# Performance work log

Measured on AMD Instinct MI355X. Metric: run time of the kernel, lower is better.

## Reference

```python
import jax, jax.numpy as jnp
import numpy as np

B, T, I, H, O, L = 128, 1024, 256, 512, 256, 2


def setup_inputs() -> dict:
    key = jax.random.key(0)
    ks = jax.random.split(key, 12)
    s_in = 1.0 / np.sqrt(I)
    s_h = 1.0 / np.sqrt(H)
    return {
        "x": jax.random.normal(ks[0], (B, T, I), dtype=jnp.float32),
        "h0": jax.random.normal(ks[1], (B, H), dtype=jnp.float32),
        # layer 0: input_size -> hidden
        "W_ih0": jax.random.uniform(ks[2], (H, I), jnp.float32, -s_in, s_in),
        "b_ih0": jax.random.uniform(ks[3], (H,), jnp.float32, -s_in, s_in),
        "W_hh0": jax.random.uniform(ks[4], (H, H), jnp.float32, -s_h, s_h),
        "b_hh0": jax.random.uniform(ks[5], (H,), jnp.float32, -s_h, s_h),
        # layer 1: hidden -> hidden
        "W_ih1": jax.random.uniform(ks[6], (H, H), jnp.float32, -s_h, s_h),
        "b_ih1": jax.random.uniform(ks[7], (H,), jnp.float32, -s_h, s_h),
        "W_hh1": jax.random.uniform(ks[8], (H, H), jnp.float32, -s_h, s_h),
        "b_hh1": jax.random.uniform(ks[9], (H,), jnp.float32, -s_h, s_h),
        # output head
        "W_out": jax.random.uniform(ks[10], (O, H), jnp.float32, -s_h, s_h),
        "b_out": jax.random.uniform(ks[11], (O,), jnp.float32, -s_h, s_h),
    }


def reference(x, h0, W_ih0, b_ih0, W_hh0, b_hh0, W_ih1, b_ih1, W_hh1, b_hh1, W_out, b_out):
    """Returns Y: (B, T, O). Single hidden state h threaded through all layers,
    matching the original module's loop structure."""
    layers = ((W_ih0, b_ih0, W_hh0, b_hh0), (W_ih1, b_ih1, W_hh1, b_hh1))

    def step(h, x_t):  # h: (B,H), x_t: (B,I)
        inp = x_t
        for (Wih, bih, Whh, bhh) in layers:
            h = jnp.tanh(inp @ Wih.T + bih + h @ Whh.T + bhh)
            inp = h
        y = inp @ W_out.T + b_out  # (B, O)
        return h, y

    xs = jnp.swapaxes(x, 0, 1)  # (T, B, I)
    _, ys = jax.lax.scan(step, h0, xs)
    return jnp.swapaxes(ys, 0, 1)  # (B, T, O)
```

## Files before the change

kernel.cpp:

```cpp
#include <hip/hip_runtime.h>
#include <cstdint>
#include <cstddef>


typedef _Float16 f16;
typedef _Float16 f16x8 __attribute__((ext_vector_type(8)));
typedef float    f32x4 __attribute__((ext_vector_type(4)));

#define NB 128
#define NT 1024
#define NI 256
#define NH 512
#define NO 256
#define RD 4

#define WS_WHH0 (size_t)(0)
#define WS_W1C  (size_t)(524288)
#define WS_WOUT (size_t)(1048576)
#define WS_WIH0 (size_t)(1310720)
#define WS_BC0  (size_t)(1572864)
#define WS_B1C  (size_t)(1574912)
#define WS_BOUT (size_t)(1576960)
#define WS_H1R  (size_t)(2097152)
#define WS_H2R  (size_t)(2621440)
#define WS_FLG  (size_t)(3145728)

#define AGENT __HIP_MEMORY_SCOPE_AGENT

__device__ __forceinline__ f32x4 mfma16(f16x8 a, f16x8 b, f32x4 c) {
  return __builtin_amdgcn_mfma_f32_16x16x32_f16(a, b, c, 0, 0, 0);
}

__device__ __forceinline__ float fast_tanh(float v) {
  float a = __builtin_fabsf(v);
  float e = __expf(-2.0f * a);
  float r = (1.0f - e) * __builtin_amdgcn_rcpf(1.0f + e);
  return v < 0.0f ? -r : r;
}

__device__ __forceinline__ void poll4(int* base, int target) {
  for (;;) {
    int a = __hip_atomic_load(base,      __ATOMIC_RELAXED, AGENT);
    int b = __hip_atomic_load(base + 16, __ATOMIC_RELAXED, AGENT);
    int c = __hip_atomic_load(base + 32, __ATOMIC_RELAXED, AGENT);
    int d = __hip_atomic_load(base + 48, __ATOMIC_RELAXED, AGENT);
    if (a >= target && b >= target && c >= target && d >= target) return;
    __builtin_amdgcn_s_sleep(2);
  }
}

__global__ __launch_bounds__(256) void rnn9277_prep(
    const float* __restrict__ h0,
    const float* __restrict__ Wih0, const float* __restrict__ bih0,
    const float* __restrict__ Whh0, const float* __restrict__ bhh0,
    const float* __restrict__ Wih1, const float* __restrict__ bih1,
    const float* __restrict__ Whh1, const float* __restrict__ bhh1,
    const float* __restrict__ Woutp, const float* __restrict__ boutp,
    char* __restrict__ ws)
{
  const int tid = blockIdx.x * 256 + threadIdx.x;
  const int stride = gridDim.x * 256;
  f16* whh0 = (f16*)(ws + WS_WHH0);
  f16* w1c  = (f16*)(ws + WS_W1C);
  f16* wout = (f16*)(ws + WS_WOUT);
  f16* wih0 = (f16*)(ws + WS_WIH0);
  float* bc0 = (float*)(ws + WS_BC0);
  float* b1c = (float*)(ws + WS_B1C);
  float* bo  = (float*)(ws + WS_BOUT);
  uint64_t* h2r64 = (uint64_t*)(ws + WS_H2R);
  int* h1f = (int*)(ws + WS_FLG);
  int* h2f = (int*)(ws + WS_FLG + 2048);

  for (int i = tid; i < NH * NH; i += stride) whh0[i] = (f16)Whh0[i];
  for (int i = tid; i < NH * NH; i += stride) w1c[i]  = (f16)(Wih1[i] + Whh1[i]);
  for (int i = tid; i < NO * NH; i += stride) wout[i] = (f16)Woutp[i];
  for (int i = tid; i < NH * NI; i += stride) wih0[i] = (f16)Wih0[i];
  for (int i = tid; i < NH; i += stride) { bc0[i] = bih0[i] + bhh0[i]; b1c[i] = bih1[i] + bhh1[i]; }
  for (int i = tid; i < NO; i += stride) bo[i] = boutp[i];
  for (int c = tid; c < NB * NH / 4; c += stride) {
    int b = c >> 7, c4 = c & 127;
    int g = b >> 4, bl = b & 15;
    const float* hp = h0 + (size_t)b * NH + c4 * 4;
    union { uint64_t u; f16 h[4]; } uv;
    uv.h[0] = (f16)hp[0]; uv.h[1] = (f16)hp[1]; uv.h[2] = (f16)hp[2]; uv.h[3] = (f16)hp[3];
    __hip_atomic_store(h2r64 + (size_t)(g * RD + 3) * 2048 + bl * 128 + c4, uv.u,
                       __ATOMIC_RELAXED, AGENT);
  }
  if (tid < 32) {
    __hip_atomic_store(h1f + tid * 16, 0, __ATOMIC_RELAXED, AGENT);
    __hip_atomic_store(h2f + tid * 16, 0, __ATOMIC_RELAXED, AGENT);
  }
}

__global__ __launch_bounds__(512) void rnn9277_chain(
    const float* __restrict__ x, float* __restrict__ out, char* __restrict__ ws)
{
  const int wg = blockIdx.x;
  const bool isL0 = wg < 32;
  const int g = (wg & 31) >> 2, j = wg & 3;
  const int tid = threadIdx.x;
  const int wave = tid >> 6, lane = tid & 63;
  const int row16 = lane & 15, kq = lane >> 4;

  const f16* whh0 = (const f16*)(ws + WS_WHH0);
  const f16* w1c  = (const f16*)(ws + WS_W1C);
  const f16* wout = (const f16*)(ws + WS_WOUT);
  const f16* wih0 = (const f16*)(ws + WS_WIH0);
  const float* bc0 = (const float*)(ws + WS_BC0);
  const float* b1c = (const float*)(ws + WS_B1C);
  const float* bo  = (const float*)(ws + WS_BOUT);
  uint64_t* h1r64 = (uint64_t*)(ws + WS_H1R);
  uint64_t* h2r64 = (uint64_t*)(ws + WS_H2R);
  int* h1fb = (int*)(ws + WS_FLG) + g * 64;
  int* h2fb = (int*)(ws + WS_FLG + 2048) + g * 64;

  __shared__ __align__(16) f16 stage[2][16 * 520];
  __shared__ __align__(16) f16 xpose[16 * 136];

  f16x8 Bh[16];
  f16x8 Bx[8];
  f16x8 By[16];
  float bias = 0.f, ybias = 0.f;
  {
    const int col = j * 128 + wave * 16 + row16;
    const f16* wp = (isL0 ? whh0 : w1c) + (size_t)col * NH + kq * 8;
    #pragma unroll
    for (int kk = 0; kk < 16; kk++) Bh[kk] = *(const f16x8*)(wp + kk * 32);
    bias = (isL0 ? bc0 : b1c)[col];
    if (isL0) {
      const f16* qp = wih0 + (size_t)col * NI + kq * 8;
      #pragma unroll
      for (int kk = 0; kk < 8; kk++) Bx[kk] = *(const f16x8*)(qp + kk * 32);
      if (wave < 4) {
        const int oc = j * 64 + wave * 16 + row16;
        const f16* rp = wout + (size_t)oc * NH + kq * 8;
        #pragma unroll
        for (int kk = 0; kk < 16; kk++) By[kk] = *(const f16x8*)(rp + kk * 32);
        ybias = bo[oc];
      }
    }
  }

  if (isL0) {
    for (int t = 0; t <= NT; ++t) {
      f32x4 acc = {0.f, 0.f, 0.f, 0.f};
      if (t < NT) {
        const float* xp = x + ((size_t)(g * 16 + row16) * NT + t) * NI + kq * 8;
        #pragma unroll
        for (int kk = 0; kk < 8; kk++) {
          f32x4 lo = *(const f32x4*)(xp + kk * 32);
          f32x4 hi = *(const f32x4*)(xp + kk * 32 + 4);
          f16x8 a;
          a[0] = (f16)lo[0]; a[1] = (f16)lo[1]; a[2] = (f16)lo[2]; a[3] = (f16)lo[3];
          a[4] = (f16)hi[0]; a[5] = (f16)hi[1]; a[6] = (f16)hi[2]; a[7] = (f16)hi[3];
          acc = mfma16(a, Bx[kk], acc);
        }
      }
      if (tid < 64) poll4(h2fb, t);
      __syncthreads();
      const uint64_t* rs = h2r64 + (size_t)(g * RD + ((t + 3) & 3)) * 2048;
      f16* st = &stage[t & 1][0];
      #pragma unroll
      for (int i = 0; i < 4; ++i) {
        int c = tid + i * 512;
        int r = c >> 7, c4 = c & 127;
        uint64_t v = __hip_atomic_load(rs + c, __ATOMIC_RELAXED, AGENT);
        *(uint64_t*)(st + r * 520 + c4 * 4) = v;
      }
      __syncthreads();

      const f16* ap = st + row16 * 520 + kq * 8;
      if (t < NT) {
        #pragma unroll
        for (int kk = 0; kk < 16; kk++)
          acc = mfma16(*(const f16x8*)(ap + kk * 32), Bh[kk], acc);
        const int cl = wave * 16 + row16;
        #pragma unroll
        for (int rr = 0; rr < 4; rr++)
          xpose[(kq * 4 + rr) * 136 + cl] = (f16)fast_tanh(acc[rr] + bias);
        __syncthreads();
        {
          int r = tid >> 5, c4 = tid & 31;
          uint64_t v = *(const uint64_t*)(xpose + r * 136 + c4 * 4);
          __hip_atomic_store(h1r64 + (size_t)(g * RD + (t & 3)) * 2048 + r * 128 + j * 32 + c4,
                             v, __ATOMIC_RELAXED, AGENT);
        }
        __syncthreads();
        if (tid == 0)
          __hip_atomic_store(h1fb + j * 16, t + 1, __ATOMIC_RELAXED, AGENT);
      }
      if (t > 0 && wave < 4) {
        f32x4 ya = {0.f, 0.f, 0.f, 0.f};
        #pragma unroll
        for (int kk = 0; kk < 16; kk++)
          ya = mfma16(*(const f16x8*)(ap + kk * 32), By[kk], ya);
        const int oc = j * 64 + wave * 16 + row16;
        #pragma unroll
        for (int rr = 0; rr < 4; rr++)
          out[((size_t)(g * 16 + kq * 4 + rr) * NT + (t - 1)) * NO + oc] = ya[rr] + ybias;
      }
    }
  } else {
    for (int t = 0; t < NT; ++t) {
      if (tid < 64) poll4(h1fb, t + 1);
      __syncthreads();
      const uint64_t* rs = h1r64 + (size_t)(g * RD + (t & 3)) * 2048;
      f16* st = &stage[t & 1][0];
      #pragma unroll
      for (int i = 0; i < 4; ++i) {
        int c = tid + i * 512;
        int r = c >> 7, c4 = c & 127;
        uint64_t v = __hip_atomic_load(rs + c, __ATOMIC_RELAXED, AGENT);
        *(uint64_t*)(st + r * 520 + c4 * 4) = v;
      }
      __syncthreads();

      const f16* ap = st + row16 * 520 + kq * 8;
      f32x4 acc = {0.f, 0.f, 0.f, 0.f};
      #pragma unroll
      for (int kk = 0; kk < 16; kk++)
        acc = mfma16(*(const f16x8*)(ap + kk * 32), Bh[kk], acc);
      const int cl = wave * 16 + row16;
      #pragma unroll
      for (int rr = 0; rr < 4; rr++)
        xpose[(kq * 4 + rr) * 136 + cl] = (f16)fast_tanh(acc[rr] + bias);
      __syncthreads();
      {
        int r = tid >> 5, c4 = tid & 31;
        uint64_t v = *(const uint64_t*)(xpose + r * 136 + c4 * 4);
        __hip_atomic_store(h2r64 + (size_t)(g * RD + (t & 3)) * 2048 + r * 128 + j * 32 + c4,
                           v, __ATOMIC_RELAXED, AGENT);
      }
      __syncthreads();
      if (tid == 0)
        __hip_atomic_store(h2fb + j * 16, t + 1, __ATOMIC_RELAXED, AGENT);
    }
  }
}

extern "C" void kernel_launch(void* const* d_in, const int* in_sizes, int n_in,
                              void* d_out, int out_size, void* d_ws, size_t ws_size,
                              hipStream_t stream) {
  const float* x    = (const float*)d_in[0];
  const float* h0   = (const float*)d_in[1];
  const float* Wih0 = (const float*)d_in[2];
  const float* bih0 = (const float*)d_in[3];
  const float* Whh0 = (const float*)d_in[4];
  const float* bhh0 = (const float*)d_in[5];
  const float* Wih1 = (const float*)d_in[6];
  const float* bih1 = (const float*)d_in[7];
  const float* Whh1 = (const float*)d_in[8];
  const float* bhh1 = (const float*)d_in[9];
  const float* Wout = (const float*)d_in[10];
  const float* bout = (const float*)d_in[11];
  char* ws = (char*)d_ws;
  float* out = (float*)d_out;

  rnn9277_prep<<<dim3(128), dim3(256), 0, stream>>>(
      h0, Wih0, bih0, Whh0, bhh0, Wih1, bih1, Whh1, bhh1, Wout, bout, ws);
  rnn9277_chain<<<dim3(64), dim3(512), 0, stream>>>(x, out, ws);
}
```

Measured before the change: 6.251 ms.

## Replace flag-based handoff with tag-embedded hidden-state panels and per-thread polling

```diff
diff --git a/kernel.cpp b/kernel.cpp
--- a/kernel.cpp
+++ b/kernel.cpp
@@ -12,7 +12,6 @@
 #define NI 256
 #define NH 512
 #define NO 256
-#define RD 4
 
 #define WS_WHH0 (size_t)(0)
 #define WS_W1C  (size_t)(524288)
@@ -21,11 +20,11 @@
 #define WS_BC0  (size_t)(1572864)
 #define WS_B1C  (size_t)(1574912)
 #define WS_BOUT (size_t)(1576960)
-#define WS_H1R  (size_t)(2097152)
-#define WS_H2R  (size_t)(2621440)
-#define WS_FLG  (size_t)(3145728)
+#define WS_H1P  (size_t)(2097152)
+#define WS_H2P  (size_t)(2621440)
 
 #define AGENT __HIP_MEMORY_SCOPE_AGENT
+#define SPIN_BUDGET (1 << 24)
 
 __device__ __forceinline__ f32x4 mfma16(f16x8 a, f16x8 b, f32x4 c) {
   return __builtin_amdgcn_mfma_f32_16x16x32_f16(a, b, c, 0, 0, 0);
@@ -38,14 +37,25 @@
   return v < 0.0f ? -r : r;
 }
 
-__device__ __forceinline__ void poll4(int* base, int target) {
+__device__ __forceinline__ uint32_t pack_h(float v, uint32_t tag) {
+  union { f16 h; uint16_t u; } cv;
+  cv.h = (f16)v;
+  return ((uint32_t)cv.u << 16) | tag;
+}
+
+__device__ __forceinline__ void poll16(uint32_t* __restrict__ panel, int tid,
+                                       uint32_t expect, uint32_t w[16],
+                                       int* budget) {
   for (;;) {
-    int a = __hip_atomic_load(base,      __ATOMIC_RELAXED, AGENT);
-    int b = __hip_atomic_load(base + 16, __ATOMIC_RELAXED, AGENT);
-    int c = __hip_atomic_load(base + 32, __ATOMIC_RELAXED, AGENT);
-    int d = __hip_atomic_load(base + 48, __ATOMIC_RELAXED, AGENT);
-    if (a >= target && b >= target && c >= target && d >= target) return;
-    __builtin_amdgcn_s_sleep(2);
+    bool ok = true;
+    #pragma unroll
+    for (int i = 0; i < 16; i++) ok &= ((w[i] & 0xFFFFu) == expect);
+    if (ok) return;
+    if (--(*budget) < 0) return;
+    __builtin_amdgcn_s_sleep(1);
+    #pragma unroll
+    for (int i = 0; i < 16; i++)
+      w[i] = __hip_atomic_load(panel + tid + i * 512, __ATOMIC_RELAXED, AGENT);
   }
 }
 
@@ -67,9 +77,8 @@
   float* bc0 = (float*)(ws + WS_BC0);
   float* b1c = (float*)(ws + WS_B1C);
   float* bo  = (float*)(ws + WS_BOUT);
-  uint64_t* h2r64 = (uint64_t*)(ws + WS_H2R);
-  int* h1f = (int*)(ws + WS_FLG);
-  int* h2f = (int*)(ws + WS_FLG + 2048);
+  uint32_t* h1p = (uint32_t*)(ws + WS_H1P);
+  uint32_t* h2p = (uint32_t*)(ws + WS_H2P);
 
   for (int i = tid; i < NH * NH; i += stride) whh0[i] = (f16)Whh0[i];
   for (int i = tid; i < NH * NH; i += stride) w1c[i]  = (f16)(Wih1[i] + Whh1[i]);
@@ -77,18 +86,16 @@
   for (int i = tid; i < NH * NI; i += stride) wih0[i] = (f16)Wih0[i];
   for (int i = tid; i < NH; i += stride) { bc0[i] = bih0[i] + bhh0[i]; b1c[i] = bih1[i] + bhh1[i]; }
   for (int i = tid; i < NO; i += stride) bo[i] = boutp[i];
-  for (int c = tid; c < NB * NH / 4; c += stride) {
-    int b = c >> 7, c4 = c & 127;
-    int g = b >> 4, bl = b & 15;
-    const float* hp = h0 + (size_t)b * NH + c4 * 4;
-    union { uint64_t u; f16 h[4]; } uv;
-    uv.h[0] = (f16)hp[0]; uv.h[1] = (f16)hp[1]; uv.h[2] = (f16)hp[2]; uv.h[3] = (f16)hp[3];
-    __hip_atomic_store(h2r64 + (size_t)(g * RD + 3) * 2048 + bl * 128 + c4, uv.u,
-                       __ATOMIC_RELAXED, AGENT);
-  }
-  if (tid < 32) {
-    __hip_atomic_store(h1f + tid * 16, 0, __ATOMIC_RELAXED, AGENT);
-    __hip_atomic_store(h2f + tid * 16, 0, __ATOMIC_RELAXED, AGENT);
+
+  for (int i = tid; i < 8 * 8192; i += stride)
+    __hip_atomic_store(h1p + i, 0u, __ATOMIC_RELAXED, AGENT);
+  for (int i = tid; i < NB * NH; i += stride) {
+    int b = i >> 9, c = i & 511;
+    int g = b >> 4, r = b & 15;
+    union { f16 h; uint16_t u; } cv;
+    cv.h = (f16)h0[i];
+    __hip_atomic_store(h2p + (size_t)g * 8192 + r * 512 + c,
+                       (uint32_t)cv.u << 16, __ATOMIC_RELAXED, AGENT);
   }
 }
 
@@ -109,13 +116,12 @@
   const float* bc0 = (const float*)(ws + WS_BC0);
   const float* b1c = (const float*)(ws + WS_B1C);
   const float* bo  = (const float*)(ws + WS_BOUT);
-  uint64_t* h1r64 = (uint64_t*)(ws + WS_H1R);
-  uint64_t* h2r64 = (uint64_t*)(ws + WS_H2R);
-  int* h1fb = (int*)(ws + WS_FLG) + g * 64;
-  int* h2fb = (int*)(ws + WS_FLG + 2048) + g * 64;
+  uint32_t* h1p = (uint32_t*)(ws + WS_H1P) + (size_t)g * 8192;
+  uint32_t* h2p = (uint32_t*)(ws + WS_H2P) + (size_t)g * 8192;
 
   __shared__ __align__(16) f16 stage[2][16 * 520];
-  __shared__ __align__(16) f16 xpose[16 * 136];
+
+  int budget = SPIN_BUDGET;
 
   f16x8 Bh[16];
   f16x8 Bx[8];
@@ -143,7 +149,12 @@
 
   if (isL0) {
     for (int t = 0; t <= NT; ++t) {
-      f32x4 acc = {0.f, 0.f, 0.f, 0.f};
+      uint32_t w[16];
+      #pragma unroll
+      for (int i = 0; i < 16; i++)
+        w[i] = __hip_atomic_load(h2p + tid + i * 512, __ATOMIC_RELAXED, AGENT);
+
+      f32x4 accx = {0.f, 0.f, 0.f, 0.f};
       if (t < NT) {
         const float* xp = x + ((size_t)(g * 16 + row16) * NT + t) * NI + kq * 8;
         #pragma unroll
@@ -153,41 +164,37 @@
           f16x8 a;
           a[0] = (f16)lo[0]; a[1] = (f16)lo[1]; a[2] = (f16)lo[2]; a[3] = (f16)lo[3];
           a[4] = (f16)hi[0]; a[5] = (f16)hi[1]; a[6] = (f16)hi[2]; a[7] = (f16)hi[3];
-          acc = mfma16(a, Bx[kk], acc);
+          accx = mfma16(a, Bx[kk], accx);
         }
       }
-      if (tid < 64) poll4(h2fb, t);
-      __syncthreads();
-      const uint64_t* rs = h2r64 + (size_t)(g * RD + ((t + 3) & 3)) * 2048;
+
+      poll16(h2p, tid, (uint32_t)t, w, &budget);
+
       f16* st = &stage[t & 1][0];
       #pragma unroll
-      for (int i = 0; i < 4; ++i) {
-        int c = tid + i * 512;
-        int r = c >> 7, c4 = c & 127;
-        uint64_t v = __hip_atomic_load(rs + c, __ATOMIC_RELAXED, AGENT);
-        *(uint64_t*)(st + r * 520 + c4 * 4) = v;
+      for (int i = 0; i < 16; i++) {
+        union { uint16_t u; f16 h; } cv;
+        cv.u = (uint16_t)(w[i] >> 16);
+        st[i * 520 + tid] = cv.h;
       }
       __syncthreads();
 
       const f16* ap = st + row16 * 520 + kq * 8;
       if (t < NT) {
-        #pragma unroll
-        for (int kk = 0; kk < 16; kk++)
-          acc = mfma16(*(const f16x8*)(ap + kk * 32), Bh[kk], acc);
-        const int cl = wave * 16 + row16;
-        #pragma unroll
-        for (int rr = 0; rr < 4; rr++)
-          xpose[(kq * 4 + rr) * 136 + cl] = (f16)fast_tanh(acc[rr] + bias);
-        __syncthreads();
-        {
-          int r = tid >> 5, c4 = tid & 31;
-          uint64_t v = *(const uint64_t*)(xpose + r * 136 + c4 * 4);
-          __hip_atomic_store(h1r64 + (size_t)(g * RD + (t & 3)) * 2048 + r * 128 + j * 32 + c4,
-                             v, __ATOMIC_RELAXED, AGENT);
+        f32x4 acc2 = {0.f, 0.f, 0.f, 0.f};
+        #pragma unroll
+        for (int kk = 0; kk < 16; kk += 2) {
+          accx = mfma16(*(const f16x8*)(ap + kk * 32), Bh[kk], accx);
+          acc2 = mfma16(*(const f16x8*)(ap + (kk + 1) * 32), Bh[kk + 1], acc2);
         }
-        __syncthreads();
-        if (tid == 0)
-          __hip_atomic_store(h1fb + j * 16, t + 1, __ATOMIC_RELAXED, AGENT);
+        const int col = j * 128 + wave * 16 + row16;
+        const uint32_t tag = (uint32_t)(t + 1);
+        #pragma unroll
+        for (int rr = 0; rr < 4; rr++) {
+          uint32_t wv = pack_h(fast_tanh(accx[rr] + acc2[rr] + bias), tag);
+          __hip_atomic_store(h1p + (kq * 4 + rr) * 512 + col, wv,
+                             __ATOMIC_RELAXED, AGENT);
+        }
       }
       if (t > 0 && wave < 4) {
         f32x4 ya = {0.f, 0.f, 0.f, 0.f};
@@ -202,38 +209,37 @@
     }
   } else {
     for (int t = 0; t < NT; ++t) {
-      if (tid < 64) poll4(h1fb, t + 1);
+      uint32_t w[16];
+      #pragma unroll
+      for (int i = 0; i < 16; i++)
+        w[i] = __hip_atomic_load(h1p + tid + i * 512, __ATOMIC_RELAXED, AGENT);
+
+      poll16(h1p, tid, (uint32_t)(t + 1), w, &budget);
+
+      f16* st = &stage[t & 1][0];
+      #pragma unroll
+      for (int i = 0; i < 16; i++) {
+        union { uint16_t u; f16 h; } cv;
+        cv.u = (uint16_t)(w[i] >> 16);
+        st[i * 520 + tid] = cv.h;
+      }
       __syncthreads();
-      const uint64_t* rs = h1r64 + (size_t)(g * RD + (t & 3)) * 2048;
-      f16* st = &stage[t & 1][0];
-      #pragma unroll
-      for (int i = 0; i < 4; ++i) {
-        int c = tid + i * 512;
-        int r = c >> 7, c4 = c & 127;
-        uint64_t v = __hip_atomic_load(rs + c, __ATOMIC_RELAXED, AGENT);
-        *(uint64_t*)(st + r * 520 + c4 * 4) = v;
-      }
-      __syncthreads();
 
       const f16* ap = st + row16 * 520 + kq * 8;
-      f32x4 acc = {0.f, 0.f, 0.f, 0.f};
-      #pragma unroll
-      for (int kk = 0; kk < 16; kk++)
-        acc = mfma16(*(const f16x8*)(ap + kk * 32), Bh[kk], acc);
-      const int cl = wave * 16 + row16;
-      #pragma unroll
-      for (int rr = 0; rr < 4; rr++)
-        xpose[(kq * 4 + rr) * 136 + cl] = (f16)fast_tanh(acc[rr] + bias);
-      __syncthreads();
-      {
-        int r = tid >> 5, c4 = tid & 31;
-        uint64_t v = *(const uint64_t*)(xpose + r * 136 + c4 * 4);
-        __hip_atomic_store(h2r64 + (size_t)(g * RD + (t & 3)) * 2048 + r * 128 + j * 32 + c4,
-                           v, __ATOMIC_RELAXED, AGENT);
-      }
-      __syncthreads();
-      if (tid == 0)
-        __hip_atomic_store(h2fb + j * 16, t + 1, __ATOMIC_RELAXED, AGENT);
+      f32x4 a0 = {0.f, 0.f, 0.f, 0.f}, a1 = {0.f, 0.f, 0.f, 0.f};
+      #pragma unroll
+      for (int kk = 0; kk < 16; kk += 2) {
+        a0 = mfma16(*(const f16x8*)(ap + kk * 32), Bh[kk], a0);
+        a1 = mfma16(*(const f16x8*)(ap + (kk + 1) * 32), Bh[kk + 1], a1);
+      }
+      const int col = j * 128 + wave * 16 + row16;
+      const uint32_t tag = (uint32_t)(t + 1);
+      #pragma unroll
+      for (int rr = 0; rr < 4; rr++) {
+        uint32_t wv = pack_h(fast_tanh(a0[rr] + a1[rr] + bias), tag);
+        __hip_atomic_store(h2p + (kq * 4 + rr) * 512 + col, wv,
+                           __ATOMIC_RELAXED, AGENT);
+      }
     }
   }
 }
```

Result: slower. 6.702 ms (+7.2%).

## Poll flags per-thread, swizzle staging LDS, store hidden state directly, split MFMA chains

Applied to the files above, without the earlier changes.

```diff
diff --git a/kernel.cpp b/kernel.cpp
--- a/kernel.cpp
+++ b/kernel.cpp
@@ -26,6 +26,7 @@
 #define WS_FLG  (size_t)(3145728)
 
 #define AGENT __HIP_MEMORY_SCOPE_AGENT
+#define SPIN_BUDGET (1 << 22)
 
 __device__ __forceinline__ f32x4 mfma16(f16x8 a, f16x8 b, f32x4 c) {
   return __builtin_amdgcn_mfma_f32_16x16x32_f16(a, b, c, 0, 0, 0);
@@ -38,14 +39,31 @@
   return v < 0.0f ? -r : r;
 }
 
-__device__ __forceinline__ void poll4(int* base, int target) {
+__device__ __forceinline__ void drain_vm() {
+  asm volatile("s_waitcnt vmcnt(0)" ::: "memory");
+}
+
+__device__ __forceinline__ void poll4(int* base, int target, int* budget) {
   for (;;) {
     int a = __hip_atomic_load(base,      __ATOMIC_RELAXED, AGENT);
     int b = __hip_atomic_load(base + 16, __ATOMIC_RELAXED, AGENT);
     int c = __hip_atomic_load(base + 32, __ATOMIC_RELAXED, AGENT);
     int d = __hip_atomic_load(base + 48, __ATOMIC_RELAXED, AGENT);
-    if (a >= target && b >= target && c >= target && d >= target) return;
-    __builtin_amdgcn_s_sleep(2);
+    if (a >= target && b >= target && c >= target && d >= target) break;
+    if (--(*budget) < 0) break;
+    __builtin_amdgcn_s_sleep(1);
+  }
+  asm volatile("" ::: "memory");
+}
+
+__device__ __forceinline__ void stage_sw(const uint64_t* rs, int tid, f16* st) {
+  #pragma unroll
+  for (int i = 0; i < 4; ++i) {
+    int cc = tid + i * 512;
+    int r = cc >> 7, c4 = cc & 127;
+    uint64_t v = __hip_atomic_load(rs + cc, __ATOMIC_RELAXED, AGENT);
+    int f = r * 512 + (((c4 >> 1) ^ (r & 7)) << 3) + ((c4 & 1) << 2);
+    *(uint64_t*)(st + f) = v;
   }
 }
 
@@ -101,6 +119,8 @@
   const int tid = threadIdx.x;
   const int wave = tid >> 6, lane = tid & 63;
   const int row16 = lane & 15, kq = lane >> 4;
+  const int khi = (row16 >> 2) & 1;
+  const int kql = (kq ^ (row16 & 3)) << 3;
 
   const f16* whh0 = (const f16*)(ws + WS_WHH0);
   const f16* w1c  = (const f16*)(ws + WS_W1C);
@@ -114,8 +134,9 @@
   int* h1fb = (int*)(ws + WS_FLG) + g * 64;
   int* h2fb = (int*)(ws + WS_FLG + 2048) + g * 64;
 
-  __shared__ __align__(16) f16 stage[2][16 * 520];
-  __shared__ __align__(16) f16 xpose[16 * 136];
+  __shared__ __align__(16) f16 stage[2][16 * 512];
+
+  int budget = SPIN_BUDGET;
 
   f16x8 Bh[16];
   f16x8 Bx[8];
@@ -143,7 +164,7 @@
 
   if (isL0) {
     for (int t = 0; t <= NT; ++t) {
-      f32x4 acc = {0.f, 0.f, 0.f, 0.f};
+      f32x4 accx = {0.f, 0.f, 0.f, 0.f};
       if (t < NT) {
         const float* xp = x + ((size_t)(g * 16 + row16) * NT + t) * NI + kq * 8;
         #pragma unroll
@@ -153,38 +174,31 @@
           f16x8 a;
           a[0] = (f16)lo[0]; a[1] = (f16)lo[1]; a[2] = (f16)lo[2]; a[3] = (f16)lo[3];
           a[4] = (f16)hi[0]; a[5] = (f16)hi[1]; a[6] = (f16)hi[2]; a[7] = (f16)hi[3];
-          acc = mfma16(a, Bx[kk], acc);
+          accx = mfma16(a, Bx[kk], accx);
         }
       }
-      if (tid < 64) poll4(h2fb, t);
+      poll4(h2fb, t, &budget);
+      stage_sw(h2r64 + (size_t)(g * RD + ((t + 3) & 3)) * 2048, tid, &stage[t & 1][0]);
       __syncthreads();
-      const uint64_t* rs = h2r64 + (size_t)(g * RD + ((t + 3) & 3)) * 2048;
-      f16* st = &stage[t & 1][0];
-      #pragma unroll
-      for (int i = 0; i < 4; ++i) {
-        int c = tid + i * 512;
-        int r = c >> 7, c4 = c & 127;
-        uint64_t v = __hip_atomic_load(rs + c, __ATOMIC_RELAXED, AGENT);
-        *(uint64_t*)(st + r * 520 + c4 * 4) = v;
-      }
-      __syncthreads();
-
-      const f16* ap = st + row16 * 520 + kq * 8;
+
+      const f16* ap = &stage[t & 1][0] + row16 * 512 + kql;
       if (t < NT) {
-        #pragma unroll
-        for (int kk = 0; kk < 16; kk++)
-          acc = mfma16(*(const f16x8*)(ap + kk * 32), Bh[kk], acc);
-        const int cl = wave * 16 + row16;
-        #pragma unroll
-        for (int rr = 0; rr < 4; rr++)
-          xpose[(kq * 4 + rr) * 136 + cl] = (f16)fast_tanh(acc[rr] + bias);
-        __syncthreads();
-        {
-          int r = tid >> 5, c4 = tid & 31;
-          uint64_t v = *(const uint64_t*)(xpose + r * 136 + c4 * 4);
-          __hip_atomic_store(h1r64 + (size_t)(g * RD + (t & 3)) * 2048 + r * 128 + j * 32 + c4,
-                             v, __ATOMIC_RELAXED, AGENT);
+        f32x4 acc2 = {0.f, 0.f, 0.f, 0.f};
+        #pragma unroll
+        for (int kk = 0; kk < 16; kk += 2) {
+          accx = mfma16(*(const f16x8*)(ap + ((kk ^ khi) << 5)),       Bh[kk],     accx);
+          acc2 = mfma16(*(const f16x8*)(ap + (((kk + 1) ^ khi) << 5)), Bh[kk + 1], acc2);
         }
+        uint16_t* pan = (uint16_t*)(h1r64 + (size_t)(g * RD + (t & 3)) * 2048);
+        const int col = j * 128 + wave * 16 + row16;
+        #pragma unroll
+        for (int rr = 0; rr < 4; rr++) {
+          union { f16 h; uint16_t u; } cv;
+          cv.h = (f16)fast_tanh(accx[rr] + acc2[rr] + bias);
+          __hip_atomic_store(pan + (kq * 4 + rr) * 512 + col, cv.u,
+                             __ATOMIC_RELAXED, AGENT);
+        }
+        drain_vm();
         __syncthreads();
         if (tid == 0)
           __hip_atomic_store(h1fb + j * 16, t + 1, __ATOMIC_RELAXED, AGENT);
@@ -193,7 +207,7 @@
         f32x4 ya = {0.f, 0.f, 0.f, 0.f};
         #pragma unroll
         for (int kk = 0; kk < 16; kk++)
-          ya = mfma16(*(const f16x8*)(ap + kk * 32), By[kk], ya);
+          ya = mfma16(*(const f16x8*)(ap + ((kk ^ khi) << 5)), By[kk], ya);
         const int oc = j * 64 + wave * 16 + row16;
         #pragma unroll
         for (int rr = 0; rr < 4; rr++)
@@ -202,35 +216,27 @@
     }
   } else {
     for (int t = 0; t < NT; ++t) {
-      if (tid < 64) poll4(h1fb, t + 1);
+      poll4(h1fb, t + 1, &budget);
+      stage_sw(h1r64 + (size_t)(g * RD + (t & 3)) * 2048, tid, &stage[t & 1][0]);
       __syncthreads();
-      const uint64_t* rs = h1r64 + (size_t)(g * RD + (t & 3)) * 2048;
-      f16* st = &stage[t & 1][0];
+
+      const f16* ap = &stage[t & 1][0] + row16 * 512 + kql;
+      f32x4 a0 = {0.f, 0.f, 0.f, 0.f}, a1 = {0.f, 0.f, 0.f, 0.f};
       #pragma unroll
-      for (int i = 0; i < 4; ++i) {
-        int c = tid + i * 512;
-        int r = c >> 7, c4 = c & 127;
-        uint64_t v = __hip_atomic_load(rs + c, __ATOMIC_RELAXED, AGENT);
-        *(uint64_t*)(st + r * 520 + c4 * 4) = v;
-      }
-      __syncthreads();
-
-      const f16* ap = st + row16 * 520 + kq * 8;
-      f32x4 acc = {0.f, 0.f, 0.f, 0.f};
+      for (int kk = 0; kk < 16; kk += 2) {
+        a0 = mfma16(*(const f16x8*)(ap + ((kk ^ khi) << 5)),       Bh[kk],     a0);
+        a1 = mfma16(*(const f16x8*)(ap + (((kk + 1) ^ khi) << 5)), Bh[kk + 1], a1);
+      }
+      uint16_t* pan = (uint16_t*)(h2r64 + (size_t)(g * RD + (t & 3)) * 2048);
+      const int col = j * 128 + wave * 16 + row16;
       #pragma unroll
-      for (int kk = 0; kk < 16; kk++)
-        acc = mfma16(*(const f16x8*)(ap + kk * 32), Bh[kk], acc);
-      const int cl = wave * 16 + row16;
-      #pragma unroll
-      for (int rr = 0; rr < 4; rr++)
-        xpose[(kq * 4 + rr) * 136 + cl] = (f16)fast_tanh(acc[rr] + bias);
-      __syncthreads();
-      {
-        int r = tid >> 5, c4 = tid & 31;
-        uint64_t v = *(const uint64_t*)(xpose + r * 136 + c4 * 4);
-        __hip_atomic_store(h2r64 + (size_t)(g * RD + (t & 3)) * 2048 + r * 128 + j * 32 + c4,
-                           v, __ATOMIC_RELAXED, AGENT);
-      }
+      for (int rr = 0; rr < 4; rr++) {
+        union { f16 h; uint16_t u; } cv;
+        cv.h = (f16)fast_tanh(a0[rr] + a1[rr] + bias);
+        __hip_atomic_store(pan + (kq * 4 + rr) * 512 + col, cv.u,
+                           __ATOMIC_RELAXED, AGENT);
+      }
+      drain_vm();
       __syncthreads();
       if (tid == 0)
         __hip_atomic_store(h2fb + j * 16, t + 1, __ATOMIC_RELAXED, AGENT);
```

Result: slower. 6.893 ms (+10.3%).
